# Optimization experiments

Measured on AMD Instinct MI355X. Metric: run time of the kernel, lower is better.

## Reference

```python
import jax, jax.numpy as jnp
import numpy as np


def setup_inputs() -> dict:
    key = jax.random.key(0)
    k1, k2, k3, k4, k5 = jax.random.split(key, 5)
    dim, hidden = 64, 128
    x = jax.random.normal(k1, (32, 128, 128, dim), dtype=jnp.float32)
    # torch Linear stores (out,in); we store transposed so y = x @ W + b
    W_expand = jax.random.normal(k2, (dim, hidden), dtype=jnp.float32) * (1.0 / np.sqrt(dim))
    b_expand = jax.random.normal(k3, (hidden,), dtype=jnp.float32) * 0.01
    W_restore = jax.random.normal(k4, (hidden, 1), dtype=jnp.float32) * (1.0 / np.sqrt(hidden))
    b_restore = jax.random.normal(k5, (1,), dtype=jnp.float32) * 0.01
    return {
        "x": x,
        "W_expand": W_expand,
        "b_expand": b_expand,
        "W_restore": W_restore,
        "b_restore": b_restore,
        "kernel_size": 2,
        "stride": 2,
    }


def reference(x, W_expand, b_expand, W_restore, b_restore, kernel_size, stride):
    b, r, c, d = x.shape
    sr = (r - kernel_size) // stride + 1
    sc = (c - kernel_size) // stride + 1
    s = stride  # original code slices stride x stride windows
    # gather all windows at once: (b, sr, s, sc, s, d)
    ri = (jnp.arange(sr) * stride)[:, None] + jnp.arange(s)[None, :]
    ci = (jnp.arange(sc) * stride)[:, None] + jnp.arange(s)[None, :]
    win = x[:, ri[:, :, None, None], ci[None, None, :, :], :]
    # -> (b, sr, sc, s*s, d)
    win = win.transpose(0, 1, 3, 2, 4, 5).reshape(b, sr, sc, s * s, d)
    # tiny MLP attention weights per window element
    h = jnp.tanh(jnp.einsum('bqpwd,dh->bqpwh', win, W_expand) + b_expand)
    logit = jax.nn.sigmoid(jnp.einsum('bqpwh,ho->bqpwo', h, W_restore)[..., 0] + b_restore[0])
    w = jax.nn.softmax(logit, axis=-1)  # over window elements
    out = jnp.sum(win * w[..., None], axis=3)  # (b, sr, sc, d)
    return out
```

## Files before the change

### kernel.cpp

```cpp
#include <hip/hip_runtime.h>


typedef __attribute__((ext_vector_type(8))) short short8;
typedef __attribute__((ext_vector_type(4))) float floatx4;

#define B_   32
#define R_   128
#define C_   128
#define D_   64
#define H_   128
#define NW_  (B_ * 64 * 64)
#define NGRP_ (NW_ / 4)
#define NBLK_ 1024
#define NWAVE_ (NBLK_ * 4)
#define L_   (NGRP_ / NWAVE_)

#define XSTEP_ (4L * R_ * C_ * D_)
#define OSTEP_ ((long)NWAVE_ * 4 * 64)

#define L2E_  1.4426950408889634f
#define T2L_  2.8853900817779268f

__device__ __forceinline__ unsigned short f2bf_rne(float f) {
  union { float f; unsigned int u; } v; v.f = f;
  unsigned int u = v.u;
  u += 0x7fffu + ((u >> 16) & 1u);
  return (unsigned short)(u >> 16);
}

__device__ __forceinline__ unsigned int pk_bf16(float lo, float hi) {
  unsigned int a = __builtin_bit_cast(unsigned int, lo) + 0x8000u;
  unsigned int b = __builtin_bit_cast(unsigned int, hi) + 0x8000u;
  return __builtin_amdgcn_perm(b, a, 0x07060302u);
}

template <int CTRL>
__device__ __forceinline__ float dpp_add(float x) {
  int xi = __builtin_bit_cast(int, x);
  int yi = __builtin_amdgcn_update_dpp(0, xi, CTRL, 0xf, 0xf, true);
  return x + __builtin_bit_cast(float, yi);
}
#define DPP_XOR1   0xB1
#define DPP_XOR3   0x1B
#define DPP_XOR7   0x141
#define DPP_XOR15  0x140
__device__ __forceinline__ float row_reduce16(float x) {
  x = dpp_add<DPP_XOR1>(x);
  x = dpp_add<DPP_XOR3>(x);
  x = dpp_add<DPP_XOR7>(x);
  x = dpp_add<DPP_XOR15>(x);
  return x;
}

__global__ void prep_kernel(const float* __restrict__ We,
                            unsigned short* __restrict__ F)
{
  int t = blockIdx.x * 256 + threadIdx.x;
  int j    = t & 7;
  int lane = (t >> 3) & 63;
  int fi   = t >> 9;
  int n  = fi >> 1, ks = fi & 1;
  int quad = lane >> 4, c = lane & 15;
  F[t] = f2bf_rne(We[(ks * 32 + quad * 8 + j) * 128 + n * 16 + c]);
}

__global__ __launch_bounds__(256, 2) void softpool_kernel(
    const float* __restrict__ x, const unsigned short* __restrict__ F,
    const float* __restrict__ be, const float* __restrict__ Wr,
    const float* __restrict__ br, float* __restrict__ out)
{
  const int lane = threadIdx.x & 63;
  const int wv   = threadIdx.x >> 6;
  const int c    = lane & 15;
  const int quad = lane >> 4;

  short8 Bf[8][2];
#pragma unroll
  for (int n = 0; n < 8; ++n)
#pragma unroll
    for (int ks = 0; ks < 2; ++ks)
      Bf[n][ks] = *(const short8*)&F[((n * 2 + ks) * 64 + lane) * 8];

  float beK[8], wr2[8], swr = 0.f;
#pragma unroll
  for (int n = 0; n < 8; ++n) {
    float w = Wr[n * 16 + c];
    beK[n] = be[n * 16 + c] * T2L_;
    wr2[n] = -2.0f * w;
    swr += w;
  }
  const float brN = -L2E_ * br[0];

  const int gw = blockIdx.x * 4 + wv;

  const int w0   = gw * 4 + (c >> 2);
  const int elem = c & 3;
  const int bb = w0 >> 12;
  const int qq = (w0 >> 6) & 63;
  const int pp = w0 & 63;
  const float* xp = x + (((bb * R_ + (qq * 2 + (elem >> 1))) * C_
                          + (pp * 2 + (elem & 1))) * D_) + quad * 8;

  const int wq0 = gw * 4 + quad;
  const int b2 = wq0 >> 12;
  const int q2 = (wq0 >> 6) & 63;
  const int p2i = wq0 & 63;
  const float* xw = x + (((b2 * R_ + q2 * 2) * C_ + p2i * 2) * D_) + c * 4;
  float* op = out + (long)wq0 * 64 + c * 4;

  floatx4 a0 = *(const floatx4*)(xp);
  floatx4 a1 = *(const floatx4*)(xp + 4);
  floatx4 a2 = *(const floatx4*)(xp + 32);
  floatx4 a3 = *(const floatx4*)(xp + 36);
  floatx4 x0 = *(const floatx4*)(xw);
  floatx4 x1 = *(const floatx4*)(xw + D_);
  floatx4 x2 = *(const floatx4*)(xw + C_ * D_);
  floatx4 x3 = *(const floatx4*)(xw + C_ * D_ + D_);

  for (int it = 0; it < L_; ++it) {
    const long nd = (it < L_ - 1) ? XSTEP_ : 0;
    const float* xpn = xp + nd;
    const float* xwn = xw + nd;
    floatx4 na0 = *(const floatx4*)(xpn);
    floatx4 na1 = *(const floatx4*)(xpn + 4);
    floatx4 na2 = *(const floatx4*)(xpn + 32);
    floatx4 na3 = *(const floatx4*)(xpn + 36);
    floatx4 nx0 = *(const floatx4*)(xwn);
    floatx4 nx1 = *(const floatx4*)(xwn + D_);
    floatx4 nx2 = *(const floatx4*)(xwn + C_ * D_);
    floatx4 nx3 = *(const floatx4*)(xwn + C_ * D_ + D_);

    union { unsigned int u[4]; short8 v; } A0u, A1u;
    A0u.u[0] = pk_bf16(a0[0], a0[1]); A0u.u[1] = pk_bf16(a0[2], a0[3]);
    A0u.u[2] = pk_bf16(a1[0], a1[1]); A0u.u[3] = pk_bf16(a1[2], a1[3]);
    A1u.u[0] = pk_bf16(a2[0], a2[1]); A1u.u[1] = pk_bf16(a2[2], a2[3]);
    A1u.u[2] = pk_bf16(a3[0], a3[1]); A1u.u[3] = pk_bf16(a3[2], a3[3]);

    floatx4 acc[8];
#pragma unroll
    for (int n = 0; n < 8; ++n) {
      floatx4 z = {0.f, 0.f, 0.f, 0.f};
      z = __builtin_amdgcn_mfma_f32_16x16x32_bf16(A0u.v, Bf[n][0], z, 0, 0, 0);
      acc[n] = __builtin_amdgcn_mfma_f32_16x16x32_bf16(A1u.v, Bf[n][1], z, 0, 0, 0);
    }

    float p0 = swr, p1 = swr, p2 = swr, p3 = swr;
#pragma unroll
    for (int n = 0; n < 8; ++n) {
      float e0 = __builtin_amdgcn_exp2f(fmaf(acc[n][0], T2L_, beK[n]));
      float e1 = __builtin_amdgcn_exp2f(fmaf(acc[n][1], T2L_, beK[n]));
      float e2 = __builtin_amdgcn_exp2f(fmaf(acc[n][2], T2L_, beK[n]));
      float e3 = __builtin_amdgcn_exp2f(fmaf(acc[n][3], T2L_, beK[n]));
      p0 = fmaf(wr2[n], __builtin_amdgcn_rcpf(e0 + 1.0f), p0);
      p1 = fmaf(wr2[n], __builtin_amdgcn_rcpf(e1 + 1.0f), p1);
      p2 = fmaf(wr2[n], __builtin_amdgcn_rcpf(e2 + 1.0f), p2);
      p3 = fmaf(wr2[n], __builtin_amdgcn_rcpf(e3 + 1.0f), p3);
    }
    p0 = row_reduce16(p0);
    p1 = row_reduce16(p1);
    p2 = row_reduce16(p2);
    p3 = row_reduce16(p3);
    float l0 = __builtin_amdgcn_rcpf(1.0f + __builtin_amdgcn_exp2f(fmaf(p0, -L2E_, brN)));
    float l1 = __builtin_amdgcn_rcpf(1.0f + __builtin_amdgcn_exp2f(fmaf(p1, -L2E_, brN)));
    float l2 = __builtin_amdgcn_rcpf(1.0f + __builtin_amdgcn_exp2f(fmaf(p2, -L2E_, brN)));
    float l3 = __builtin_amdgcn_rcpf(1.0f + __builtin_amdgcn_exp2f(fmaf(p3, -L2E_, brN)));
    float s0 = __builtin_amdgcn_exp2f(l0 * L2E_);
    float s1 = __builtin_amdgcn_exp2f(l1 * L2E_);
    float s2 = __builtin_amdgcn_exp2f(l2 * L2E_);
    float s3 = __builtin_amdgcn_exp2f(l3 * L2E_);
    float inv = __builtin_amdgcn_rcpf(s0 + s1 + s2 + s3);
    float w0f = s0 * inv, w1f = s1 * inv, w2f = s2 * inv, w3f = s3 * inv;

    floatx4 o = x0 * w0f + x1 * w1f + x2 * w2f + x3 * w3f;
    *(floatx4*)(op) = o;

    xp = xpn; xw = xwn; op += OSTEP_;
    a0 = na0; a1 = na1; a2 = na2; a3 = na3;
    x0 = nx0; x1 = nx1; x2 = nx2; x3 = nx3;
  }
}

extern "C" void kernel_launch(void* const* d_in, const int* in_sizes, int n_in,
                              void* d_out, int out_size, void* d_ws, size_t ws_size,
                              hipStream_t stream) {
  const float* x  = (const float*)d_in[0];
  const float* We = (const float*)d_in[1];
  const float* be = (const float*)d_in[2];
  const float* Wr = (const float*)d_in[3];
  const float* br = (const float*)d_in[4];
  float* out = (float*)d_out;
  unsigned short* F = (unsigned short*)d_ws;

  prep_kernel<<<32, 256, 0, stream>>>(We, F);
  softpool_kernel<<<NBLK_, 256, 0, stream>>>(x, F, be, Wr, br, out);
}
```

Before: 210.1 us.

## Reuse MFMA operand loads for weighted sum and deepen prefetch to two iterations

Drops the second global read of each window (the xw loads) and builds the weighted output from the fp32 values already loaded for the MFMA A-operand. Each lane's softmax weight is fetched with ds_bpermute, and partial products are reduced across lanes with DPP quad sums. The prefetch becomes a 3-stage register ring that loads two iterations ahead, and the loop is fully unrolled. This halves redundant global/L2 traffic per window and adds latency hiding, at the cost of more DPP/bpermute ALU work and higher register pressure.

```diff
diff --git a/kernel.cpp b/kernel.cpp
--- a/kernel.cpp
+++ b/kernel.cpp
@@ -41,6 +41,7 @@
   return x + __builtin_bit_cast(float, yi);
 }
 #define DPP_XOR1   0xB1
+#define DPP_XOR2   0x4E
 #define DPP_XOR3   0x1B
 #define DPP_XOR7   0x141
 #define DPP_XOR15  0x140
@@ -49,6 +50,11 @@
   x = dpp_add<DPP_XOR3>(x);
   x = dpp_add<DPP_XOR7>(x);
   x = dpp_add<DPP_XOR15>(x);
+  return x;
+}
+__device__ __forceinline__ float quad_sum(float x) {
+  x = dpp_add<DPP_XOR1>(x);
+  x = dpp_add<DPP_XOR2>(x);
   return x;
 }
 
@@ -101,34 +107,38 @@
   const float* xp = x + (((bb * R_ + (qq * 2 + (elem >> 1))) * C_
                           + (pp * 2 + (elem & 1))) * D_) + quad * 8;
 
-  const int wq0 = gw * 4 + quad;
-  const int b2 = wq0 >> 12;
-  const int q2 = (wq0 >> 6) & 63;
-  const int p2i = wq0 & 63;
-  const float* xw = x + (((b2 * R_ + q2 * 2) * C_ + p2i * 2) * D_) + c * 4;
-  float* op = out + (long)wq0 * 64 + c * 4;
-
-  floatx4 a0 = *(const floatx4*)(xp);
-  floatx4 a1 = *(const floatx4*)(xp + 4);
-  floatx4 a2 = *(const floatx4*)(xp + 32);
-  floatx4 a3 = *(const floatx4*)(xp + 36);
-  floatx4 x0 = *(const floatx4*)(xw);
-  floatx4 x1 = *(const floatx4*)(xw + D_);
-  floatx4 x2 = *(const floatx4*)(xw + C_ * D_);
-  floatx4 x3 = *(const floatx4*)(xw + C_ * D_ + D_);
-
+  const int win = c >> 2;
+  float* op = out + (long)(gw * 4 + win) * 64
+            + quad * 8 + ((elem & 1) << 2) + ((elem & 2) << 4);
+
+  const int  widx = (win * 16 + elem) << 2;
+  const bool oddc = (c & 1) != 0;
+  const bool hi2c = (c & 2) != 0;
+
+  floatx4 st[3][4];
+#pragma unroll
+  for (int s = 0; s < 2; ++s) {
+    const float* p = xp + (long)s * XSTEP_;
+    st[s][0] = *(const floatx4*)(p);
+    st[s][1] = *(const floatx4*)(p + 4);
+    st[s][2] = *(const floatx4*)(p + 32);
+    st[s][3] = *(const floatx4*)(p + 36);
+  }
+
+#pragma unroll
   for (int it = 0; it < L_; ++it) {
-    const long nd = (it < L_ - 1) ? XSTEP_ : 0;
-    const float* xpn = xp + nd;
-    const float* xwn = xw + nd;
-    floatx4 na0 = *(const floatx4*)(xpn);
-    floatx4 na1 = *(const floatx4*)(xpn + 4);
-    floatx4 na2 = *(const floatx4*)(xpn + 32);
-    floatx4 na3 = *(const floatx4*)(xpn + 36);
-    floatx4 nx0 = *(const floatx4*)(xwn);
-    floatx4 nx1 = *(const floatx4*)(xwn + D_);
-    floatx4 nx2 = *(const floatx4*)(xwn + C_ * D_);
-    floatx4 nx3 = *(const floatx4*)(xwn + C_ * D_ + D_);
+    if (it < L_ - 2) {
+      const int ps = (it + 2) % 3;
+      const float* p = xp + 2 * XSTEP_;
+      st[ps][0] = *(const floatx4*)(p);
+      st[ps][1] = *(const floatx4*)(p + 4);
+      st[ps][2] = *(const floatx4*)(p + 32);
+      st[ps][3] = *(const floatx4*)(p + 36);
+    }
+
+    const int cs = it % 3;
+    const floatx4 a0 = st[cs][0], a1 = st[cs][1];
+    const floatx4 a2 = st[cs][2], a3 = st[cs][3];
 
     union { unsigned int u[4]; short8 v; } A0u, A1u;
     A0u.u[0] = pk_bf16(a0[0], a0[1]); A0u.u[1] = pk_bf16(a0[2], a0[3]);
@@ -171,12 +181,26 @@
     float inv = __builtin_amdgcn_rcpf(s0 + s1 + s2 + s3);
     float w0f = s0 * inv, w1f = s1 * inv, w2f = s2 * inv, w3f = s3 * inv;
 
-    floatx4 o = x0 * w0f + x1 * w1f + x2 * w2f + x3 * w3f;
+    float wa = oddc ? w1f : w0f;
+    float wb = oddc ? w3f : w2f;
+    float wsel = hi2c ? wb : wa;
+    float W = __builtin_bit_cast(float,
+        __builtin_amdgcn_ds_bpermute(widx, __builtin_bit_cast(int, wsel)));
+
+    floatx4 t0 = a0 * W, t1 = a1 * W, t2 = a2 * W, t3 = a3 * W;
+    floatx4 o0, o1, o2, o3;
+#pragma unroll
+    for (int j = 0; j < 4; ++j) {
+      o0[j] = quad_sum(t0[j]);
+      o1[j] = quad_sum(t1[j]);
+      o2[j] = quad_sum(t2[j]);
+      o3[j] = quad_sum(t3[j]);
+    }
+    floatx4 o = hi2c ? (oddc ? o3 : o2) : (oddc ? o1 : o0);
     *(floatx4*)(op) = o;
 
-    xp = xpn; xw = xwn; op += OSTEP_;
-    a0 = na0; a1 = na1; a2 = na2; a3 = na3;
-    x0 = nx0; x1 = nx1; x2 = nx2; x3 = nx3;
+    xp += XSTEP_;
+    op += OSTEP_;
   }
 }
 
```

Measured after the change: 209.5 us. No clear change (-0.3%).
